# Optimization experiments

Hardware: AMD Instinct MI355X
Metric: run time of the kernel (lower is better)

The kernel has to match this reference:

```python
import jax, jax.numpy as jnp
import numpy as np

B, H, SQ, SKV, D = 2, 16, 2048, 2048, 128
EMBED_DIM = H * D  # 2048; temperature init = embedding_dim // num_heads = 128


def setup_inputs() -> dict:
    key = jax.random.key(0)
    kq, kk, kv = jax.random.split(key, 3)
    query = jax.random.normal(kq, (B, H, SQ, D), dtype=jnp.float32)
    k = jax.random.normal(kk, (B, H, SKV, D), dtype=jnp.float32)
    value = jax.random.normal(kv, (B, H, SKV, D), dtype=jnp.float32)
    # learnable per-head temperature, initialized to embedding_dim // num_heads
    temperature = jnp.ones((1, H, 1, 1), dtype=jnp.float32) * (EMBED_DIM // H)
    return {"query": query, "key": k, "value": value, "temperature": temperature}


def reference(query, key, value, temperature):
    # qk = Q @ K^T  -> [B, H, Sq, Skv]
    qk = jnp.einsum("bhqd,bhkd->bhqk", query, key)
    scaled_qk = qk * (1.0 / temperature)  # per-head learnable inverse scale
    attn = jax.nn.softmax(scaled_qk, axis=-1)
    # dropout is identity in eval / p=0
    out = jnp.einsum("bhqk,bhkd->bhqd", attn, value)
    return out
```

## Files before the change

### kernel.cpp

```cpp
#include <hip/hip_runtime.h>
#include <cstdint>
#include <cstddef>

#define BB 2
#define HH 16
#define SQ 2048
#define SKV 2048
#define DD 128

#define QT 128
#define KT 64
#define NT (SKV / KT)
#define KSTR 136
#define VSTR 72
#define KBUF (64 * KSTR)
#define VBUF (128 * VSTR)

typedef __attribute__((ext_vector_type(8))) short short8;
typedef __attribute__((ext_vector_type(16))) float floatx16;

#define LDS_BARRIER() asm volatile("s_waitcnt lgkmcnt(0)\n\ts_barrier" ::: "memory")

__device__ __forceinline__ unsigned short f2bf(float f) {
    union { float f; unsigned u; } x;
    x.f = f;
    unsigned r = x.u + 0x7fffu + ((x.u >> 16) & 1u);
    return (unsigned short)(r >> 16);
}

__device__ __forceinline__ unsigned cvt_pk_bf16(float a, float b) {
    unsigned r;
    asm("v_cvt_pk_bf16_f32 %0, %1, %2" : "=v"(r) : "v"(a), "v"(b));
    return r;
}

__global__ __launch_bounds__(256) void conv_k_kernel(const float* __restrict__ K,
                                                     unsigned short* __restrict__ Kb)
{
    size_t idx = ((size_t)blockIdx.x * 256 + threadIdx.x) * 8;
    float4 a = *(const float4*)(K + idx);
    float4 b = *(const float4*)(K + idx + 4);
    short8 o;
    o[0] = (short)f2bf(a.x); o[1] = (short)f2bf(a.y);
    o[2] = (short)f2bf(a.z); o[3] = (short)f2bf(a.w);
    o[4] = (short)f2bf(b.x); o[5] = (short)f2bf(b.y);
    o[6] = (short)f2bf(b.z); o[7] = (short)f2bf(b.w);
    *(short8*)(Kb + idx) = o;
}

__global__ __launch_bounds__(256) void trans_v_kernel(const float* __restrict__ V,
                                                      unsigned short* __restrict__ Vtb)
{
    __shared__ __align__(16) unsigned short lds[DD * VSTR];
    const int tid = threadIdx.x;
    const int kvt = blockIdx.x;
    const int bh  = blockIdx.y;

    const float* Vp = V + ((size_t)bh * SKV + (size_t)kvt * KT) * DD;
#pragma unroll
    for (int it = 0; it < 8; ++it) {
        int f4   = it * 256 + tid;
        int row  = f4 >> 5;
        int prow = (row & ~12) | ((row & 4) << 1) | ((row & 8) >> 1);
        int col4 = (f4 & 31) << 2;
        float4 v = *(const float4*)(Vp + (size_t)row * DD + col4);
        lds[(col4 + 0) * VSTR + prow] = f2bf(v.x);
        lds[(col4 + 1) * VSTR + prow] = f2bf(v.y);
        lds[(col4 + 2) * VSTR + prow] = f2bf(v.z);
        lds[(col4 + 3) * VSTR + prow] = f2bf(v.w);
    }
    __syncthreads();
#pragma unroll
    for (int it = 0; it < 4; ++it) {
        int idx = it * 256 + tid;
        int d   = idx >> 3;
        int c8  = (idx & 7) << 3;
        short8 s = *(const short8*)&lds[d * VSTR + c8];
        *(short8*)(Vtb + ((size_t)bh * DD + d) * SKV + (size_t)kvt * KT + c8) = s;
    }
}

__global__ __launch_bounds__(256, 2) void fattn_kernel(
    const float* __restrict__ Q, const unsigned short* __restrict__ Kb,
    const unsigned short* __restrict__ Vtb, const float* __restrict__ T,
    float* __restrict__ O)
{
    __shared__ __align__(16) unsigned short lds_k[2][KBUF];
    __shared__ __align__(16) unsigned short lds_v[2][VBUF];

    const int tid  = threadIdx.x;
    const int wave = tid >> 6;
    const int lane = tid & 63;
    const int l31  = lane & 31;
    const int hi   = lane >> 5;

    const int wg    = blockIdx.x;
    const int bh    = (wg & 7) * 4 + ((wg >> 3) & 3);
    const int qtile = wg >> 5;
    const int h     = bh & (HH - 1);

    const float scale = 1.44269504088896f / T[h];

    const float*          Qp  = Q   + (size_t)bh * SQ * DD;
    const unsigned short* Kp  = Kb  + (size_t)bh * SKV * DD;
    const unsigned short* Vtp = Vtb + (size_t)bh * DD * SKV;
    float*                Op  = O   + (size_t)bh * SQ * DD;

    short8 qf[8];
    {
        const int qrow = qtile * QT + wave * 32 + l31;
#pragma unroll
        for (int ks = 0; ks < 8; ++ks) {
            const float* p = Qp + (size_t)qrow * DD + ks * 16 + hi * 8;
            float4 a = *(const float4*)(p);
            float4 b = *(const float4*)(p + 4);
            short8 q;
            q[0] = (short)f2bf(a.x * scale); q[1] = (short)f2bf(a.y * scale);
            q[2] = (short)f2bf(a.z * scale); q[3] = (short)f2bf(a.w * scale);
            q[4] = (short)f2bf(b.x * scale); q[5] = (short)f2bf(b.y * scale);
            q[6] = (short)f2bf(b.z * scale); q[7] = (short)f2bf(b.w * scale);
            qf[ks] = q;
        }
    }

    floatx16 oacc[4];
#pragma unroll
    for (int dt = 0; dt < 4; ++dt)
#pragma unroll
        for (int r = 0; r < 16; ++r) oacc[dt][r] = 0.f;
    float psum = 0.f;

    const int kcr = tid >> 4;
    const int kcc = (tid & 15) << 3;
    const int vcr = tid >> 3;
    const int vcc = (tid & 7) << 3;

    short8 kp[4], vp[4];

#define LOADT(t) do { \
        const unsigned short* kt_ = Kp + (size_t)(t) * KT * DD; \
        const unsigned short* vt_ = Vtp + (size_t)(t) * KT; \
        kp[0] = *(const short8*)(kt_ + (size_t)(kcr     ) * DD + kcc); \
        kp[1] = *(const short8*)(kt_ + (size_t)(kcr + 16) * DD + kcc); \
        kp[2] = *(const short8*)(kt_ + (size_t)(kcr + 32) * DD + kcc); \
        kp[3] = *(const short8*)(kt_ + (size_t)(kcr + 48) * DD + kcc); \
        vp[0] = *(const short8*)(vt_ + (size_t)(vcr     ) * SKV + vcc); \
        vp[1] = *(const short8*)(vt_ + (size_t)(vcr + 32) * SKV + vcc); \
        vp[2] = *(const short8*)(vt_ + (size_t)(vcr + 64) * SKV + vcc); \
        vp[3] = *(const short8*)(vt_ + (size_t)(vcr + 96) * SKV + vcc); \
    } while (0)

#define STAGET(buf) do { \
        *(short8*)&lds_k[buf][(kcr     ) * KSTR + kcc] = kp[0]; \
        *(short8*)&lds_k[buf][(kcr + 16) * KSTR + kcc] = kp[1]; \
        *(short8*)&lds_k[buf][(kcr + 32) * KSTR + kcc] = kp[2]; \
        *(short8*)&lds_k[buf][(kcr + 48) * KSTR + kcc] = kp[3]; \
        *(short8*)&lds_v[buf][(vcr     ) * VSTR + vcc] = vp[0]; \
        *(short8*)&lds_v[buf][(vcr + 32) * VSTR + vcc] = vp[1]; \
        *(short8*)&lds_v[buf][(vcr + 64) * VSTR + vcc] = vp[2]; \
        *(short8*)&lds_v[buf][(vcr + 96) * VSTR + vcc] = vp[3]; \
    } while (0)

    LOADT(0);
    STAGET(0);
    LOADT(1);
    LDS_BARRIER();

    for (int t = 0; t < NT; ++t) {
        const int cur = t & 1;
        const unsigned short* lk = lds_k[cur];
        const unsigned short* lv = lds_v[cur];

        floatx16 s0, s1;
#pragma unroll
        for (int r = 0; r < 16; ++r) { s0[r] = 0.f; s1[r] = 0.f; }
        __builtin_amdgcn_s_setprio(1);
#pragma unroll
        for (int ks = 0; ks < 8; ++ks) {
            short8 kf0 = *(const short8*)&lk[(l31     ) * KSTR + ks * 16 + hi * 8];
            short8 kf1 = *(const short8*)&lk[(l31 + 32) * KSTR + ks * 16 + hi * 8];
            s0 = __builtin_amdgcn_mfma_f32_32x32x16_bf16(kf0, qf[ks], s0, 0, 0, 0);
            s1 = __builtin_amdgcn_mfma_f32_32x32x16_bf16(kf1, qf[ks], s1, 0, 0, 0);
        }
        __builtin_amdgcn_s_setprio(0);

        unsigned pk0[8], pk1[8];
#pragma unroll
        for (int i = 0; i < 8; ++i) {
            float e0 = __builtin_amdgcn_exp2f(s0[2 * i]);
            float e1 = __builtin_amdgcn_exp2f(s0[2 * i + 1]);
            float e2 = __builtin_amdgcn_exp2f(s1[2 * i]);
            float e3 = __builtin_amdgcn_exp2f(s1[2 * i + 1]);
            psum += (e0 + e1) + (e2 + e3);
            pk0[i] = cvt_pk_bf16(e0, e1);
            pk1[i] = cvt_pk_bf16(e2, e3);
        }
        union { unsigned u[4]; short8 s8; } ap[2][2];
#pragma unroll
        for (int w = 0; w < 4; ++w) {
            ap[0][0].u[w] = pk0[w];
            ap[0][1].u[w] = pk0[w + 4];
            ap[1][0].u[w] = pk1[w];
            ap[1][1].u[w] = pk1[w + 4];
        }

        if (t + 1 < NT) STAGET(cur ^ 1);

        __builtin_amdgcn_s_setprio(1);
#pragma unroll
        for (int kvt = 0; kvt < 2; ++kvt)
#pragma unroll
            for (int s = 0; s < 2; ++s) {
                const int cb = kvt * 32 + s * 16 + hi * 8;
#pragma unroll
                for (int dt = 0; dt < 4; ++dt) {
                    short8 vf = *(const short8*)&lv[(dt * 32 + l31) * VSTR + cb];
                    oacc[dt] = __builtin_amdgcn_mfma_f32_32x32x16_bf16(
                        ap[kvt][s].s8, vf, oacc[dt], 0, 0, 0);
                }
            }
        __builtin_amdgcn_s_setprio(0);

        if (t + 2 < NT) LOADT(t + 2);

        LDS_BARRIER();
    }

    float tot = psum + __shfl_xor(psum, 32, 64);
    float inv = 1.0f / tot;
    float ivr[16];
#pragma unroll
    for (int r = 0; r < 16; ++r) {
        const int ql = (r & 3) + 8 * (r >> 2) + 4 * hi;
        ivr[r] = __shfl(inv, ql, 64);
    }
    const int qbase = qtile * QT + wave * 32;
#pragma unroll
    for (int dt = 0; dt < 4; ++dt)
#pragma unroll
        for (int r = 0; r < 16; ++r) {
            const int ql = (r & 3) + 8 * (r >> 2) + 4 * hi;
            Op[(size_t)(qbase + ql) * DD + dt * 32 + l31] = oacc[dt][r] * ivr[r];
        }
#undef LOADT
#undef STAGET
}

extern "C" void kernel_launch(void* const* d_in, const int* in_sizes, int n_in,
                              void* d_out, int out_size, void* d_ws, size_t ws_size,
                              hipStream_t stream) {
    const float* Q = (const float*)d_in[0];
    const float* K = (const float*)d_in[1];
    const float* V = (const float*)d_in[2];
    const float* T = (const float*)d_in[3];
    float* O = (float*)d_out;

    unsigned short* Kb  = (unsigned short*)d_ws;
    unsigned short* Vtb = Kb + (size_t)BB * HH * SKV * DD;

    const size_t nK = (size_t)BB * HH * SKV * DD;
    conv_k_kernel<<<dim3(nK / (256 * 8)), 256, 0, stream>>>(K, Kb);
    trans_v_kernel<<<dim3(SKV / KT, BB * HH), 256, 0, stream>>>(V, Vtb);

    fattn_kernel<<<dim3((SQ / QT) * BB * HH), 256, 0, stream>>>(Q, Kb, Vtb, T, O);
}
```

Baseline: 197.8 us.

## Double per-wave query rows and interleave half-tile softmax with PV MFMAs

```diff
diff --git a/kernel.cpp b/kernel.cpp
--- a/kernel.cpp
+++ b/kernel.cpp
@@ -8,7 +8,7 @@
 #define SKV 2048
 #define DD 128
 
-#define QT 128
+#define QT 256
 #define KT 64
 #define NT (SKV / KT)
 #define KSTR 136
@@ -80,7 +80,7 @@
     }
 }
 
-__global__ __launch_bounds__(256, 2) void fattn_kernel(
+__global__ __launch_bounds__(256, 1) void fattn_kernel(
     const float* __restrict__ Q, const unsigned short* __restrict__ Kb,
     const unsigned short* __restrict__ Vtb, const float* __restrict__ T,
     float* __restrict__ O)
@@ -106,9 +106,10 @@
     const unsigned short* Vtp = Vtb + (size_t)bh * DD * SKV;
     float*                Op  = O   + (size_t)bh * SQ * DD;
 
-    short8 qf[8];
-    {
-        const int qrow = qtile * QT + wave * 32 + l31;
+    short8 qf[2][8];
+#pragma unroll
+    for (int m = 0; m < 2; ++m) {
+        const int qrow = qtile * QT + wave * 64 + m * 32 + l31;
 #pragma unroll
         for (int ks = 0; ks < 8; ++ks) {
             const float* p = Qp + (size_t)qrow * DD + ks * 16 + hi * 8;
@@ -119,16 +120,18 @@
             q[2] = (short)f2bf(a.z * scale); q[3] = (short)f2bf(a.w * scale);
             q[4] = (short)f2bf(b.x * scale); q[5] = (short)f2bf(b.y * scale);
             q[6] = (short)f2bf(b.z * scale); q[7] = (short)f2bf(b.w * scale);
-            qf[ks] = q;
-        }
-    }
-
-    floatx16 oacc[4];
-#pragma unroll
-    for (int dt = 0; dt < 4; ++dt)
-#pragma unroll
-        for (int r = 0; r < 16; ++r) oacc[dt][r] = 0.f;
-    float psum = 0.f;
+            qf[m][ks] = q;
+        }
+    }
+
+    floatx16 oacc[2][4];
+#pragma unroll
+    for (int m = 0; m < 2; ++m)
+#pragma unroll
+        for (int dt = 0; dt < 4; ++dt)
+#pragma unroll
+            for (int r = 0; r < 16; ++r) oacc[m][dt][r] = 0.f;
+    float psum[2] = {0.f, 0.f};
 
     const int kcr = tid >> 4;
     const int kcc = (tid & 15) << 3;
@@ -171,77 +174,118 @@
         const unsigned short* lk = lds_k[cur];
         const unsigned short* lv = lds_v[cur];
 
-        floatx16 s0, s1;
-#pragma unroll
-        for (int r = 0; r < 16; ++r) { s0[r] = 0.f; s1[r] = 0.f; }
+        floatx16 s[2][2];
+#pragma unroll
+        for (int m = 0; m < 2; ++m)
+#pragma unroll
+            for (int half = 0; half < 2; ++half)
+#pragma unroll
+                for (int r = 0; r < 16; ++r) s[m][half][r] = 0.f;
         __builtin_amdgcn_s_setprio(1);
 #pragma unroll
         for (int ks = 0; ks < 8; ++ks) {
             short8 kf0 = *(const short8*)&lk[(l31     ) * KSTR + ks * 16 + hi * 8];
             short8 kf1 = *(const short8*)&lk[(l31 + 32) * KSTR + ks * 16 + hi * 8];
-            s0 = __builtin_amdgcn_mfma_f32_32x32x16_bf16(kf0, qf[ks], s0, 0, 0, 0);
-            s1 = __builtin_amdgcn_mfma_f32_32x32x16_bf16(kf1, qf[ks], s1, 0, 0, 0);
+#pragma unroll
+            for (int m = 0; m < 2; ++m) {
+                s[m][0] = __builtin_amdgcn_mfma_f32_32x32x16_bf16(kf0, qf[m][ks], s[m][0], 0, 0, 0);
+                s[m][1] = __builtin_amdgcn_mfma_f32_32x32x16_bf16(kf1, qf[m][ks], s[m][1], 0, 0, 0);
+            }
         }
         __builtin_amdgcn_s_setprio(0);
 
-        unsigned pk0[8], pk1[8];
-#pragma unroll
-        for (int i = 0; i < 8; ++i) {
-            float e0 = __builtin_amdgcn_exp2f(s0[2 * i]);
-            float e1 = __builtin_amdgcn_exp2f(s0[2 * i + 1]);
-            float e2 = __builtin_amdgcn_exp2f(s1[2 * i]);
-            float e3 = __builtin_amdgcn_exp2f(s1[2 * i + 1]);
-            psum += (e0 + e1) + (e2 + e3);
-            pk0[i] = cvt_pk_bf16(e0, e1);
-            pk1[i] = cvt_pk_bf16(e2, e3);
-        }
-        union { unsigned u[4]; short8 s8; } ap[2][2];
-#pragma unroll
-        for (int w = 0; w < 4; ++w) {
-            ap[0][0].u[w] = pk0[w];
-            ap[0][1].u[w] = pk0[w + 4];
-            ap[1][0].u[w] = pk1[w];
-            ap[1][1].u[w] = pk1[w + 4];
+        union { unsigned u[4]; short8 s8; } ap[2][2][2];
+
+#pragma unroll
+        for (int m = 0; m < 2; ++m) {
+            unsigned pk[8];
+#pragma unroll
+            for (int i = 0; i < 8; ++i) {
+                float e0 = __builtin_amdgcn_exp2f(s[m][0][2 * i]);
+                float e1 = __builtin_amdgcn_exp2f(s[m][0][2 * i + 1]);
+                psum[m] += e0 + e1;
+                pk[i] = cvt_pk_bf16(e0, e1);
+            }
+#pragma unroll
+            for (int w = 0; w < 4; ++w) {
+                ap[m][0][0].u[w] = pk[w];
+                ap[m][0][1].u[w] = pk[w + 4];
+            }
         }
 
         if (t + 1 < NT) STAGET(cur ^ 1);
 
         __builtin_amdgcn_s_setprio(1);
 #pragma unroll
-        for (int kvt = 0; kvt < 2; ++kvt)
-#pragma unroll
-            for (int s = 0; s < 2; ++s) {
-                const int cb = kvt * 32 + s * 16 + hi * 8;
-#pragma unroll
-                for (int dt = 0; dt < 4; ++dt) {
-                    short8 vf = *(const short8*)&lv[(dt * 32 + l31) * VSTR + cb];
-                    oacc[dt] = __builtin_amdgcn_mfma_f32_32x32x16_bf16(
-                        ap[kvt][s].s8, vf, oacc[dt], 0, 0, 0);
-                }
-            }
+        for (int s2 = 0; s2 < 2; ++s2) {
+            const int cb = s2 * 16 + hi * 8;
+#pragma unroll
+            for (int dt = 0; dt < 4; ++dt) {
+                short8 vf = *(const short8*)&lv[(dt * 32 + l31) * VSTR + cb];
+#pragma unroll
+                for (int m = 0; m < 2; ++m)
+                    oacc[m][dt] = __builtin_amdgcn_mfma_f32_32x32x16_bf16(
+                        ap[m][0][s2].s8, vf, oacc[m][dt], 0, 0, 0);
+            }
+        }
         __builtin_amdgcn_s_setprio(0);
 
+#pragma unroll
+        for (int m = 0; m < 2; ++m) {
+            unsigned pk[8];
+#pragma unroll
+            for (int i = 0; i < 8; ++i) {
+                float e0 = __builtin_amdgcn_exp2f(s[m][1][2 * i]);
+                float e1 = __builtin_amdgcn_exp2f(s[m][1][2 * i + 1]);
+                psum[m] += e0 + e1;
+                pk[i] = cvt_pk_bf16(e0, e1);
+            }
+#pragma unroll
+            for (int w = 0; w < 4; ++w) {
+                ap[m][1][0].u[w] = pk[w];
+                ap[m][1][1].u[w] = pk[w + 4];
+            }
+        }
+
         if (t + 2 < NT) LOADT(t + 2);
 
+        __builtin_amdgcn_s_setprio(1);
+#pragma unroll
+        for (int s2 = 0; s2 < 2; ++s2) {
+            const int cb = 32 + s2 * 16 + hi * 8;
+#pragma unroll
+            for (int dt = 0; dt < 4; ++dt) {
+                short8 vf = *(const short8*)&lv[(dt * 32 + l31) * VSTR + cb];
+#pragma unroll
+                for (int m = 0; m < 2; ++m)
+                    oacc[m][dt] = __builtin_amdgcn_mfma_f32_32x32x16_bf16(
+                        ap[m][1][s2].s8, vf, oacc[m][dt], 0, 0, 0);
+            }
+        }
+        __builtin_amdgcn_s_setprio(0);
+
         LDS_BARRIER();
     }
 
-    float tot = psum + __shfl_xor(psum, 32, 64);
-    float inv = 1.0f / tot;
-    float ivr[16];
-#pragma unroll
-    for (int r = 0; r < 16; ++r) {
-        const int ql = (r & 3) + 8 * (r >> 2) + 4 * hi;
-        ivr[r] = __shfl(inv, ql, 64);
-    }
-    const int qbase = qtile * QT + wave * 32;
-#pragma unroll
-    for (int dt = 0; dt < 4; ++dt)
+#pragma unroll
+    for (int m = 0; m < 2; ++m) {
+        float tot = psum[m] + __shfl_xor(psum[m], 32, 64);
+        float inv = 1.0f / tot;
+        float ivr[16];
 #pragma unroll
         for (int r = 0; r < 16; ++r) {
             const int ql = (r & 3) + 8 * (r >> 2) + 4 * hi;
-            Op[(size_t)(qbase + ql) * DD + dt * 32 + l31] = oacc[dt][r] * ivr[r];
-        }
+            ivr[r] = __shfl(inv, ql, 64);
+        }
+        const int qbase = qtile * QT + wave * 64 + m * 32;
+#pragma unroll
+        for (int dt = 0; dt < 4; ++dt)
+#pragma unroll
+            for (int r = 0; r < 16; ++r) {
+                const int ql = (r & 3) + 8 * (r >> 2) + 4 * hi;
+                Op[(size_t)(qbase + ql) * DD + dt * 32 + l31] = oacc[m][dt][r] * ivr[r];
+            }
+    }
 #undef LOADT
 #undef STAGET
 }
```

Result: slower. 203.4 us (+2.8%).
